# Optimization experiments

Measured on AMD Instinct MI355X. Metric: run time of the kernel, lower is better.

Reference implementation:

```python
import jax, jax.numpy as jnp
import numpy as np

H = 128  # hidden_size
DF = 6   # d_feat
T = 60
N = 8192
E = 30   # num_ind
SLOPE = 0.01  # LeakyReLU default


def leaky(v):
    return jnp.where(v >= 0, v, SLOPE * v)


def gru_layer(xs, Wih, Whh, bih, bhh):
    # xs: [T, N, D_in] -> ys: [T, N, H]
    n = xs.shape[1]
    h0 = jnp.zeros((n, H), dtype=xs.dtype)

    def step(h, xt):
        gi = xt @ Wih.T + bih          # [N, 3H]
        gh = h @ Whh.T + bhh           # [N, 3H]
        i_r, i_z, i_n = jnp.split(gi, 3, axis=1)
        h_r, h_z, h_n = jnp.split(gh, 3, axis=1)
        r = jax.nn.sigmoid(i_r + h_r)
        z = jax.nn.sigmoid(i_z + h_z)
        ncand = jnp.tanh(i_n + r * h_n)
        h_new = (1.0 - z) * ncand + z * h
        return h_new, h_new

    h_last, ys = jax.lax.scan(step, h0, xs)
    return ys, h_last


def setup_inputs() -> dict:
    key = jax.random.key(0)
    ks = jax.random.split(key, 16)
    s = 0.08
    inp = {
        "x": jax.random.normal(ks[0], (N, T, DF), dtype=jnp.float32),
        "GH": jax.random.uniform(ks[1], (N, E), dtype=jnp.float32),
        # GRU layer 0
        "Wih0": jax.random.normal(ks[2], (3 * H, DF), dtype=jnp.float32) * s,
        "Whh0": jax.random.normal(ks[3], (3 * H, H), dtype=jnp.float32) * s,
        "bih0": jax.random.normal(ks[4], (3 * H,), dtype=jnp.float32) * s,
        "bhh0": jax.random.normal(ks[5], (3 * H,), dtype=jnp.float32) * s,
        # GRU layer 1
        "Wih1": jax.random.normal(ks[6], (3 * H, H), dtype=jnp.float32) * s,
        "Whh1": jax.random.normal(ks[7], (3 * H, H), dtype=jnp.float32) * s,
        "bih1": jax.random.normal(ks[8], (3 * H,), dtype=jnp.float32) * s,
        "bhh1": jax.random.normal(ks[9], (3 * H,), dtype=jnp.float32) * s,
        # attention transformation + vector a
        "Wt": jax.random.normal(ks[10], (H, H), dtype=jnp.float32) * s,
        "bt": jax.random.normal(ks[11], (H,), dtype=jnp.float32) * s,
        "a": jax.random.normal(ks[12], (2 * H, 1), dtype=jnp.float32),
        # output heads
        "Wfc": jax.random.normal(ks[13], (H, H), dtype=jnp.float32) * s,
        "bfc": jax.random.normal(ks[14], (H,), dtype=jnp.float32) * s,
        "Wout": jax.random.normal(ks[15], (1, H), dtype=jnp.float32) * s,
        "bout": jnp.zeros((1,), dtype=jnp.float32),
    }
    return inp


def reference(x, GH, Wih0, Whh0, bih0, bhh0, Wih1, Whh1, bih1, bhh1,
              Wt, bt, a, Wfc, bfc, Wout, bout):
    # --- 2-layer GRU, batch_first; keep only last time step ---
    xs = jnp.swapaxes(x, 0, 1)                 # [T, N, DF]
    ys, _ = gru_layer(xs, Wih0, Whh0, bih0, bhh0)
    _, hidden = gru_layer(ys, Wih1, Whh1, bih1, bhh1)  # [N, H]

    # --- hyperedge aggregation ---
    hidden_agg = GH.T @ hidden                 # [E, H]

    # --- GAT-style attention, fused: score[i,j] = a1.x_i + a2.y_j ---
    xt = hidden @ Wt.T + bt                    # [N, H]
    yt = hidden_agg @ Wt.T + bt                # [E, H]
    a1 = a[:H, 0]
    a2 = a[H:, 0]
    scores = (xt @ a1)[:, None] + (yt @ a2)[None, :]   # [N, E]
    att = jax.nn.softmax(leaky(scores), axis=1)        # softmax over edges

    # --- diagonal pinv (pseudo-reciprocal); note GH.sum(1)**1/2 == sum/2 ---
    de = GH.sum(axis=0)                        # [E]
    dv = GH.sum(axis=1) / 2.0                  # [N]
    inv_de = jnp.where(de != 0, 1.0 / jnp.where(de != 0, de, 1.0), 0.0)
    inv_dv = jnp.where(dv != 0, 1.0 / jnp.where(dv != 0, dv, 1.0), 0.0)

    # H = Dv @ att @ De @ att^T @ Dv
    left = (inv_dv[:, None] * att) * inv_de[None, :]   # [N, E]
    Hmat = (left @ att.T) * inv_dv[None, :]            # [N, N]

    hidden = Hmat @ hidden + hidden
    hidden = leaky(hidden @ Wfc.T + bfc)
    out = (hidden @ Wout.T + bout).squeeze()           # [N]
    return out
```

## Files before the change

kernel.cpp:

```cpp
#include <hip/hip_runtime.h>
#include <hip/hip_fp16.h>
#include <cstddef>

#define H 128
#define E_ 30
#define T_ 60
#define DF 6

typedef unsigned int u32;
typedef __attribute__((ext_vector_type(8))) short short8;
typedef __attribute__((ext_vector_type(4))) float f32x4;

#define OFF_PACK   0
#define OFF_WFCT   79872
#define OFF_HID    96256
#define OFF_SX     1144832
#define OFF_IDV    1153024
#define OFF_AGG    1161216
#define OFF_DE     1165056
#define OFF_S      1165088
#define OFF_IDE    1168928
#define OFF_SY     1168960
#define OFF_CC     1168992
#define OFF_WV1    1169024
#define OFF_WV2    1169152
#define ZERO_CNT   7712

__device__ __forceinline__ unsigned short f2h(float f) {
    return __half_as_ushort(__float2half(f));
}

__global__ void k_pack(const float* __restrict__ Wih0, const float* __restrict__ Whh0,
                       const float* __restrict__ Wih1, const float* __restrict__ Whh1,
                       uint4* __restrict__ pack)
{
    int u = blockIdx.x * 256 + threadIdx.x;
    int lane = u & 63;
    int s = (u >> 6) % 39;
    int j = (u >> 6) / 39;
    int hc = j * 16 + (lane & 15);
    int g = lane >> 4;
    int layer, gate, kt;
    if (s < 5)       { layer = 0; gate = 0; kt = s; }
    else if (s < 10) { layer = 0; gate = 1; kt = s - 5; }
    else if (s < 14) { layer = 0; gate = 2; kt = s - 10; }
    else if (s < 15) { layer = 0; gate = 3; kt = 0; }
    else if (s < 23) { layer = 1; gate = 0; kt = s - 15; }
    else if (s < 31) { layer = 1; gate = 1; kt = s - 23; }
    else if (s < 35) { layer = 1; gate = 2; kt = s - 31; }
    else             { layer = 1; gate = 3; kt = s - 35; }

    u32 wd[4];
    for (int p = 0; p < 4; ++p) {
        unsigned short hh[2];
        for (int q = 0; q < 2; ++q) {
            int k = kt * 32 + g * 8 + p * 2 + q;
            float v = 0.f;
            if (layer == 0) {
                if (gate <= 1) {
                    int row = gate * 128 + hc;
                    if (k < 128) v = Whh0[row * 128 + k];
                    else if (k < 134) v = Wih0[row * 6 + (k - 128)];
                } else if (gate == 2) {
                    v = Whh0[(256 + hc) * 128 + k];
                } else {
                    if (k < 6) v = Wih0[(256 + hc) * 6 + k];
                }
            } else {
                if (gate <= 1) {
                    int row = gate * 128 + hc;
                    v = (k < 128) ? Wih1[row * 128 + k] : Whh1[row * 128 + (k - 128)];
                } else if (gate == 2) {
                    v = Whh1[(256 + hc) * 128 + k];
                } else {
                    v = Wih1[(256 + hc) * 128 + k];
                }
            }
            hh[q] = f2h(v);
        }
        wd[p] = (u32)hh[0] | ((u32)hh[1] << 16);
    }
    pack[(j * 39 + s) * 64 + lane] = make_uint4(wd[0], wd[1], wd[2], wd[3]);
}

__global__ void k_prep_fc(const float* __restrict__ Wfc, float* __restrict__ WfcT)
{
    int i = blockIdx.x * 256 + threadIdx.x;
    int col = i / 128, h = i % 128;
    WfcT[h * 128 + col] = Wfc[i];
}

__global__ void k_prep_wv(const float* __restrict__ Wt, const float* __restrict__ bt,
                          const float* __restrict__ a, float* __restrict__ wv1,
                          float* __restrict__ wv2, float* __restrict__ cc)
{
    int i = threadIdx.x;
    float s1 = 0.f, s2 = 0.f;
    for (int j = 0; j < H; ++j) {
        float w = Wt[(size_t)j * H + i];
        s1 += w * a[j];
        s2 += w * a[H + j];
    }
    wv1[i] = s1;
    wv2[i] = s2;
    if (i == 0) {
        float c1 = 0.f, c2 = 0.f;
        for (int j = 0; j < H; ++j) { c1 += bt[j] * a[j]; c2 += bt[j] * a[H + j]; }
        cc[0] = c1; cc[1] = c2;
    }
}

__global__ void k_zero(float* __restrict__ z)
{
    int i = blockIdx.x * 256 + threadIdx.x;
    if (i < ZERO_CNT) z[i] = 0.f;
}

#define MFMA16 __builtin_amdgcn_mfma_f32_16x16x32_f16

__global__ __launch_bounds__(512, 2) void k_gru(
    const float* __restrict__ x,
    const uint4* __restrict__ pack,
    const float* __restrict__ bih0, const float* __restrict__ bhh0,
    const float* __restrict__ bih1, const float* __restrict__ bhh1,
    float* __restrict__ hidden)
{
    extern __shared__ char smem[];
    const int tid = threadIdx.x;
    const int lane = tid & 63;
    const int j = tid >> 6;
    const int xr = lane & 15;
    const int g = lane >> 4;
    const int hc = (j << 4) + xr;
    const int n0 = blockIdx.x << 5;

    for (int c = tid; c < 32 * 60; c += 512) {
        int r = c / 60, t = c % 60;
        const float* xp = x + (size_t)(n0 + r) * (T_ * DF) + t * DF;
        u32 w0 = (u32)f2h(xp[0]) | ((u32)f2h(xp[1]) << 16);
        u32 w1 = (u32)f2h(xp[2]) | ((u32)f2h(xp[3]) << 16);
        u32 w2 = (u32)f2h(xp[4]) | ((u32)f2h(xp[5]) << 16);
        *(uint4*)(smem + 32768 + t * 512 + r * 16) = make_uint4(w0, w1, w2, 0u);
    }
    for (int i = tid; i < 384; i += 512) ((u32*)(smem + 32768 + 30720))[i] = 0u;
    for (int i = tid; i < 4096; i += 512) {
        ((u32*)smem)[i] = 0u;
        ((u32*)(smem + 16384))[i] = 0u;
    }

    uint4 wv[39];
#pragma unroll
    for (int s = 0; s < 39; ++s) wv[s] = pack[((j * 39 + s) << 6) + lane];

    const float br0 = bih0[hc] + bhh0[hc];
    const float bz0 = bih0[H + hc] + bhh0[H + hc];
    const float bgn0 = bhh0[2 * H + hc];
    const float bgi0 = bih0[2 * H + hc];
    const float br1 = bih1[hc] + bhh1[hc];
    const float bz1 = bih1[H + hc] + bhh1[H + hc];
    const float bgn1 = bhh1[2 * H + hc];
    const float bgi1 = bih1[2 * H + hc];

    float hs0[2][4] = {{0.f,0.f,0.f,0.f},{0.f,0.f,0.f,0.f}};
    float hs1[2][4] = {{0.f,0.f,0.f,0.f},{0.f,0.f,0.f,0.f}};

    const char* xbase = smem + 32768 + (g << 9) + (xr << 4);

    __syncthreads();

    for (int t = 0; t <= T_; ++t) {
        const int pr  = (t & 1) << 13;
        const int prx = pr ^ 8192;

#pragma unroll
        for (int rt = 0; rt < 2; ++rt) {
            const int R = (rt << 4) + xr;
            const int rowb = R << 8;

            uint4 f0[4];
#pragma unroll
            for (int kt = 0; kt < 4; ++kt)
                f0[kt] = *(const uint4*)(smem + prx + rowb + ((((kt << 2) | g) ^ xr) << 4));

            if (t < T_) {
                f32x4 aR = {0,0,0,0}, aZ = {0,0,0,0}, aG = {0,0,0,0}, aI = {0,0,0,0};
                uint4 fx = *(const uint4*)(xbase + (size_t)t * 512 + rt * 256);
                short8 xv = __builtin_bit_cast(short8, fx);
#pragma unroll
                for (int kt = 0; kt < 4; ++kt) {
                    short8 av = __builtin_bit_cast(short8, f0[kt]);
                    aR = MFMA16(av, __builtin_bit_cast(short8, wv[kt]), aR, 0, 0, 0);
                    aZ = MFMA16(av, __builtin_bit_cast(short8, wv[5 + kt]), aZ, 0, 0, 0);
                    aG = MFMA16(av, __builtin_bit_cast(short8, wv[10 + kt]), aG, 0, 0, 0);
                }
                aR = MFMA16(xv, __builtin_bit_cast(short8, wv[4]), aR, 0, 0, 0);
                aZ = MFMA16(xv, __builtin_bit_cast(short8, wv[9]), aZ, 0, 0, 0);
                aI = MFMA16(xv, __builtin_bit_cast(short8, wv[14]), aI, 0, 0, 0);
#pragma unroll
                for (int i = 0; i < 4; ++i) {
                    float rg = __builtin_amdgcn_rcpf(1.f + __expf(-(aR[i] + br0)));
                    float zg = __builtin_amdgcn_rcpf(1.f + __expf(-(aZ[i] + bz0)));
                    float nn = aI[i] + bgi0 + rg * (aG[i] + bgn0);
                    float e2 = __expf(2.f * nn);
                    float ng = 1.f - 2.f * __builtin_amdgcn_rcpf(e2 + 1.f);
                    float hn = ng + zg * (hs0[rt][i] - ng);
                    hs0[rt][i] = hn;
                    int Rw = (rt << 4) + (g << 2) + i;
                    *(unsigned short*)(smem + pr + (Rw << 8) + (((hc >> 3) ^ (Rw & 15)) << 4) + ((hc & 7) << 1)) = f2h(hn);
                }
            }
            __builtin_amdgcn_sched_barrier(0);

            if (t > 0) {
                f32x4 cR = {0,0,0,0}, cZ = {0,0,0,0}, cG = {0,0,0,0}, cI = {0,0,0,0};
#pragma unroll
                for (int kt = 0; kt < 4; ++kt) {
                    short8 av = __builtin_bit_cast(short8, f0[kt]);
                    cR = MFMA16(av, __builtin_bit_cast(short8, wv[15 + kt]), cR, 0, 0, 0);
                    cZ = MFMA16(av, __builtin_bit_cast(short8, wv[23 + kt]), cZ, 0, 0, 0);
                    cI = MFMA16(av, __builtin_bit_cast(short8, wv[35 + kt]), cI, 0, 0, 0);
                }
#pragma unroll
                for (int kt = 0; kt < 4; ++kt) {
                    uint4 f1 = *(const uint4*)(smem + 16384 + pr + rowb + ((((kt << 2) | g) ^ xr) << 4));
                    short8 bv = __builtin_bit_cast(short8, f1);
                    cR = MFMA16(bv, __builtin_bit_cast(short8, wv[19 + kt]), cR, 0, 0, 0);
                    cZ = MFMA16(bv, __builtin_bit_cast(short8, wv[27 + kt]), cZ, 0, 0, 0);
                    cG = MFMA16(bv, __builtin_bit_cast(short8, wv[31 + kt]), cG, 0, 0, 0);
                }
#pragma unroll
                for (int i = 0; i < 4; ++i) {
                    float rg = __builtin_amdgcn_rcpf(1.f + __expf(-(cR[i] + br1)));
                    float zg = __builtin_amdgcn_rcpf(1.f + __expf(-(cZ[i] + bz1)));
                    float nn = cI[i] + bgi1 + rg * (cG[i] + bgn1);
                    float e2 = __expf(2.f * nn);
                    float ng = 1.f - 2.f * __builtin_amdgcn_rcpf(e2 + 1.f);
                    float hn = ng + zg * (hs1[rt][i] - ng);
                    hs1[rt][i] = hn;
                    int Rw = (rt << 4) + (g << 2) + i;
                    *(unsigned short*)(smem + 16384 + prx + (Rw << 8) + (((hc >> 3) ^ (Rw & 15)) << 4) + ((hc & 7) << 1)) = f2h(hn);
                }
            }
            __builtin_amdgcn_sched_barrier(0);
        }
        __syncthreads();
    }

#pragma unroll
    for (int rt = 0; rt < 2; ++rt)
#pragma unroll
        for (int i = 0; i < 4; ++i) {
            int Rw = (rt << 4) + (g << 2) + i;
            hidden[(size_t)(n0 + Rw) * H + hc] = hs1[rt][i];
        }
}

__global__ void k_rowstats(const float* __restrict__ hidden, const float* __restrict__ GH,
                           const float* __restrict__ wv1, const float* __restrict__ cc,
                           float* __restrict__ sx, float* __restrict__ invdv)
{
    int lane = threadIdx.x & 63;
    int wv = threadIdx.x >> 6;
    int n = blockIdx.x * 4 + wv;
    float p = hidden[(size_t)n * H + lane] * wv1[lane]
            + hidden[(size_t)n * H + 64 + lane] * wv1[64 + lane];
    float g = (lane < E_) ? GH[(size_t)n * E_ + lane] : 0.f;
#pragma unroll
    for (int off = 32; off > 0; off >>= 1) {
        p += __shfl_down(p, off);
        g += __shfl_down(g, off);
    }
    if (lane == 0) {
        sx[n] = p + cc[0];
        float dv = 0.5f * g;
        invdv[n] = (dv != 0.f) ? 1.f / dv : 0.f;
    }
}

__global__ void k_agg(const float* __restrict__ hidden, const float* __restrict__ GH,
                      float* __restrict__ agg, float* __restrict__ de)
{
    int t = threadIdx.x;
    int nbase = blockIdx.x * 32;
    if (t < H) {
        float part[E_];
#pragma unroll
        for (int e = 0; e < E_; ++e) part[e] = 0.f;
        for (int r = 0; r < 32; ++r) {
            int n = nbase + r;
            float hv = hidden[(size_t)n * H + t];
#pragma unroll
            for (int e = 0; e < E_; ++e) part[e] += GH[(size_t)n * E_ + e] * hv;
        }
#pragma unroll
        for (int e = 0; e < E_; ++e) atomicAdd(&agg[e * H + t], part[e]);
    } else if (t < H + E_) {
        int e = t - H;
        float s = 0.f;
        for (int r = 0; r < 32; ++r) s += GH[(size_t)(nbase + r) * E_ + e];
        atomicAdd(&de[e], s);
    }
}

__global__ void k_sy(const float* __restrict__ agg, const float* __restrict__ wv2,
                     const float* __restrict__ cc, const float* __restrict__ de,
                     float* __restrict__ sy, float* __restrict__ invde)
{
    int e = threadIdx.x;
    if (e < E_) {
        float s = 0.f;
        for (int h = 0; h < H; ++h) s += agg[e * H + h] * wv2[h];
        sy[e] = s + cc[1];
        float d = de[e];
        invde[e] = (d != 0.f) ? 1.f / d : 0.f;
    }
}

__global__ void k_attS(const float* __restrict__ hidden, const float* __restrict__ sx,
                       const float* __restrict__ sy, const float* __restrict__ invdv,
                       float* __restrict__ S)
{
    __shared__ float att_s[32][E_];
    __shared__ float sy_s[E_];
    int t = threadIdx.x;
    if (t < E_) sy_s[t] = sy[t];
    __syncthreads();
    int nbase = blockIdx.x * 32;
    if (t < 32) {
        int n = nbase + t;
        float sxn = sx[n];
        float vv[E_];
        float m = -1e30f;
#pragma unroll
        for (int e = 0; e < E_; ++e) {
            float v = sxn + sy_s[e];
            v = (v >= 0.f) ? v : 0.01f * v;
            vv[e] = v;
            m = fmaxf(m, v);
        }
        float ss = 0.f;
#pragma unroll
        for (int e = 0; e < E_; ++e) { vv[e] = __expf(vv[e] - m); ss += vv[e]; }
        float sc = invdv[n] / ss;
#pragma unroll
        for (int e = 0; e < E_; ++e) att_s[t][e] = vv[e] * sc;
    }
    __syncthreads();
    if (t < H) {
        float part[E_];
#pragma unroll
        for (int e = 0; e < E_; ++e) part[e] = 0.f;
        for (int r = 0; r < 32; ++r) {
            float hv = hidden[(size_t)(nbase + r) * H + t];
#pragma unroll
            for (int e = 0; e < E_; ++e) part[e] += att_s[r][e] * hv;
        }
#pragma unroll
        for (int e = 0; e < E_; ++e) atomicAdd(&S[e * H + t], part[e]);
    }
}

__global__ __launch_bounds__(256) void k_final(
    const float* __restrict__ hidden, const float* __restrict__ sx,
    const float* __restrict__ sy, const float* __restrict__ invdv,
    const float* __restrict__ invde, const float* __restrict__ S,
    const float* __restrict__ WfcT, const float* __restrict__ bfc,
    const float* __restrict__ Wout, const float* __restrict__ bout,
    float* __restrict__ out)
{
    __shared__ float S_s[E_ * H];
    __shared__ float sy_s[E_], ide_s[E_];
    __shared__ float nh[4][H];
    int t = threadIdx.x;
    for (int i = t; i < E_ * H; i += 256) S_s[i] = S[i];
    if (t < E_) { sy_s[t] = sy[t]; ide_s[t] = invde[t]; }
    __syncthreads();
    int wv = t >> 6, lane = t & 63;
    float wouta = Wout[lane], woutb = Wout[64 + lane];
    float bfca = bfc[lane], bfcb = bfc[64 + lane];
    float boutv = bout[0];
    for (int it = 0; it < 8; ++it) {
        int n = blockIdx.x * 32 + it * 4 + wv;
        float sxn = sx[n];
        float idv = invdv[n];
        float vv[E_];
        float m = -1e30f;
#pragma unroll
        for (int e = 0; e < E_; ++e) {
            float v = sxn + sy_s[e];
            v = (v >= 0.f) ? v : 0.01f * v;
            vv[e] = v;
            m = fmaxf(m, v);
        }
        float ss = 0.f;
#pragma unroll
        for (int e = 0; e < E_; ++e) { vv[e] = __expf(vv[e] - m); ss += vv[e]; }
        float sc = idv / ss;
        float a0 = hidden[(size_t)n * H + lane];
        float a1 = hidden[(size_t)n * H + 64 + lane];
#pragma unroll
        for (int e = 0; e < E_; ++e) {
            float wgt = vv[e] * sc * ide_s[e];
            a0 += wgt * S_s[e * H + lane];
            a1 += wgt * S_s[e * H + 64 + lane];
        }
        nh[wv][lane] = a0;
        nh[wv][64 + lane] = a1;
        __syncthreads();
        float f0 = bfca, f1 = bfcb;
        for (int h = 0; h < H; h += 4) {
            float4 nv = *(const float4*)&nh[wv][h];
            f0 += nv.x * WfcT[(h + 0) * H + lane] + nv.y * WfcT[(h + 1) * H + lane]
                + nv.z * WfcT[(h + 2) * H + lane] + nv.w * WfcT[(h + 3) * H + lane];
            f1 += nv.x * WfcT[(h + 0) * H + 64 + lane] + nv.y * WfcT[(h + 1) * H + 64 + lane]
                + nv.z * WfcT[(h + 2) * H + 64 + lane] + nv.w * WfcT[(h + 3) * H + 64 + lane];
        }
        f0 = (f0 >= 0.f) ? f0 : 0.01f * f0;
        f1 = (f1 >= 0.f) ? f1 : 0.01f * f1;
        float op = f0 * wouta + f1 * woutb;
#pragma unroll
        for (int off = 32; off > 0; off >>= 1) op += __shfl_down(op, off);
        if (lane == 0) out[n] = op + boutv;
        __syncthreads();
    }
}

extern "C" void kernel_launch(void* const* d_in, const int* in_sizes, int n_in,
                              void* d_out, int out_size, void* d_ws, size_t ws_size,
                              hipStream_t stream)
{
    const float* x    = (const float*)d_in[0];
    const float* GH   = (const float*)d_in[1];
    const float* Wih0 = (const float*)d_in[2];
    const float* Whh0 = (const float*)d_in[3];
    const float* bih0 = (const float*)d_in[4];
    const float* bhh0 = (const float*)d_in[5];
    const float* Wih1 = (const float*)d_in[6];
    const float* Whh1 = (const float*)d_in[7];
    const float* bih1 = (const float*)d_in[8];
    const float* bhh1 = (const float*)d_in[9];
    const float* Wt   = (const float*)d_in[10];
    const float* bt   = (const float*)d_in[11];
    const float* a    = (const float*)d_in[12];
    const float* Wfc  = (const float*)d_in[13];
    const float* bfc  = (const float*)d_in[14];
    const float* Wout = (const float*)d_in[15];
    const float* bout = (const float*)d_in[16];

    float* ws    = (float*)d_ws;
    uint4* pack  = (uint4*)(ws + OFF_PACK);
    float* WfcT  = ws + OFF_WFCT;
    float* hid   = ws + OFF_HID;
    float* sx    = ws + OFF_SX;
    float* idv   = ws + OFF_IDV;
    float* agg   = ws + OFF_AGG;
    float* de    = ws + OFF_DE;
    float* S     = ws + OFF_S;
    float* ide   = ws + OFF_IDE;
    float* sy    = ws + OFF_SY;
    float* cc    = ws + OFF_CC;
    float* wv1   = ws + OFF_WV1;
    float* wv2   = ws + OFF_WV2;

    k_pack<<<78, 256, 0, stream>>>(Wih0, Whh0, Wih1, Whh1, pack);
    k_prep_fc<<<64, 256, 0, stream>>>(Wfc, WfcT);
    k_prep_wv<<<1, 128, 0, stream>>>(Wt, bt, a, wv1, wv2, cc);
    k_zero<<<31, 256, 0, stream>>>(agg);

    const size_t lds_bytes = 65024;
    (void)hipFuncSetAttribute((const void*)k_gru,
                              hipFuncAttributeMaxDynamicSharedMemorySize,
                              (int)lds_bytes);
    k_gru<<<256, 512, lds_bytes, stream>>>(x, pack, bih0, bhh0, bih1, bhh1, hid);

    k_rowstats<<<2048, 256, 0, stream>>>(hid, GH, wv1, cc, sx, idv);
    k_agg<<<256, 256, 0, stream>>>(hid, GH, agg, de);
    k_sy<<<1, 64, 0, stream>>>(agg, wv2, cc, de, sy, ide);
    k_attS<<<256, 256, 0, stream>>>(hid, sx, sy, idv, S);
    k_final<<<256, 256, 0, stream>>>(hid, sx, sy, idv, ide, S, WfcT, bfc,
                                     Wout, bout, (float*)d_out);
}
```

Before: 244.4 us.

## Pipeline GRU layers across wave roles and merge small prep/stat kernels

The GRU kernel now uses 1024 threads, split into two wave roles. One role computes layer 0 at step p together with layer 1's input projection, and the other computes layer 1 at step p-1, passing the projection through LDS. This wavefront pipeline halves the per-wave weight register footprint and overlaps the two layers' serial recurrences. The four prep kernels are merged into one launch, rowstats is folded into the aggregation kernel, and the tiny k_sy kernel is removed by recomputing sy and inv_de inside the consumers. The trade-offs are more __syncthreads per step, a larger LDS footprint, and redundant sy recomputation in every block.

```diff
diff --git a/kernel.cpp b/kernel.cpp
--- a/kernel.cpp
+++ b/kernel.cpp
@@ -19,8 +19,6 @@
 #define OFF_AGG    1161216
 #define OFF_DE     1165056
 #define OFF_S      1165088
-#define OFF_IDE    1168928
-#define OFF_SY     1168960
 #define OFF_CC     1168992
 #define OFF_WV1    1169024
 #define OFF_WV2    1169152
@@ -30,95 +28,96 @@
     return __half_as_ushort(__float2half(f));
 }
 
-__global__ void k_pack(const float* __restrict__ Wih0, const float* __restrict__ Whh0,
-                       const float* __restrict__ Wih1, const float* __restrict__ Whh1,
-                       uint4* __restrict__ pack)
+__global__ void k_prep_all(const float* __restrict__ Wih0, const float* __restrict__ Whh0,
+                           const float* __restrict__ Wih1, const float* __restrict__ Whh1,
+                           const float* __restrict__ Wfc, const float* __restrict__ Wt,
+                           const float* __restrict__ bt, const float* __restrict__ a,
+                           uint4* __restrict__ pack, float* __restrict__ WfcT,
+                           float* __restrict__ wv1, float* __restrict__ wv2,
+                           float* __restrict__ cc, float* __restrict__ zbase)
 {
-    int u = blockIdx.x * 256 + threadIdx.x;
-    int lane = u & 63;
-    int s = (u >> 6) % 39;
-    int j = (u >> 6) / 39;
-    int hc = j * 16 + (lane & 15);
-    int g = lane >> 4;
-    int layer, gate, kt;
-    if (s < 5)       { layer = 0; gate = 0; kt = s; }
-    else if (s < 10) { layer = 0; gate = 1; kt = s - 5; }
-    else if (s < 14) { layer = 0; gate = 2; kt = s - 10; }
-    else if (s < 15) { layer = 0; gate = 3; kt = 0; }
-    else if (s < 23) { layer = 1; gate = 0; kt = s - 15; }
-    else if (s < 31) { layer = 1; gate = 1; kt = s - 23; }
-    else if (s < 35) { layer = 1; gate = 2; kt = s - 31; }
-    else             { layer = 1; gate = 3; kt = s - 35; }
-
-    u32 wd[4];
-    for (int p = 0; p < 4; ++p) {
-        unsigned short hh[2];
-        for (int q = 0; q < 2; ++q) {
-            int k = kt * 32 + g * 8 + p * 2 + q;
-            float v = 0.f;
-            if (layer == 0) {
-                if (gate <= 1) {
-                    int row = gate * 128 + hc;
-                    if (k < 128) v = Whh0[row * 128 + k];
-                    else if (k < 134) v = Wih0[row * 6 + (k - 128)];
-                } else if (gate == 2) {
-                    v = Whh0[(256 + hc) * 128 + k];
+    int b = blockIdx.x;
+    if (b < 78) {
+        int u = b * 256 + threadIdx.x;
+        int lane = u & 63;
+        int s = (u >> 6) % 39;
+        int j = (u >> 6) / 39;
+        int hc = j * 16 + (lane & 15);
+        int g = lane >> 4;
+        int layer, gate, kt;
+        if (s < 5)       { layer = 0; gate = 0; kt = s; }
+        else if (s < 10) { layer = 0; gate = 1; kt = s - 5; }
+        else if (s < 14) { layer = 0; gate = 2; kt = s - 10; }
+        else if (s < 15) { layer = 0; gate = 3; kt = 0; }
+        else if (s < 23) { layer = 1; gate = 0; kt = s - 15; }
+        else if (s < 31) { layer = 1; gate = 1; kt = s - 23; }
+        else if (s < 35) { layer = 1; gate = 2; kt = s - 31; }
+        else             { layer = 1; gate = 3; kt = s - 35; }
+        u32 wd[4];
+        for (int p = 0; p < 4; ++p) {
+            unsigned short hh[2];
+            for (int q = 0; q < 2; ++q) {
+                int k = kt * 32 + g * 8 + p * 2 + q;
+                float v = 0.f;
+                if (layer == 0) {
+                    if (gate <= 1) {
+                        int row = gate * 128 + hc;
+                        if (k < 128) v = Whh0[row * 128 + k];
+                        else if (k < 134) v = Wih0[row * 6 + (k - 128)];
+                    } else if (gate == 2) {
+                        v = Whh0[(256 + hc) * 128 + k];
+                    } else {
+                        if (k < 6) v = Wih0[(256 + hc) * 6 + k];
+                    }
                 } else {
-                    if (k < 6) v = Wih0[(256 + hc) * 6 + k];
+                    if (gate <= 1) {
+                        int row = gate * 128 + hc;
+                        v = (k < 128) ? Wih1[row * 128 + k] : Whh1[row * 128 + (k - 128)];
+                    } else if (gate == 2) {
+                        v = Whh1[(256 + hc) * 128 + k];
+                    } else {
+                        v = Wih1[(256 + hc) * 128 + k];
+                    }
                 }
-            } else {
-                if (gate <= 1) {
-                    int row = gate * 128 + hc;
-                    v = (k < 128) ? Wih1[row * 128 + k] : Whh1[row * 128 + (k - 128)];
-                } else if (gate == 2) {
-                    v = Whh1[(256 + hc) * 128 + k];
-                } else {
-                    v = Wih1[(256 + hc) * 128 + k];
-                }
-            }
-            hh[q] = f2h(v);
-        }
-        wd[p] = (u32)hh[0] | ((u32)hh[1] << 16);
-    }
-    pack[(j * 39 + s) * 64 + lane] = make_uint4(wd[0], wd[1], wd[2], wd[3]);
-}
-
-__global__ void k_prep_fc(const float* __restrict__ Wfc, float* __restrict__ WfcT)
-{
-    int i = blockIdx.x * 256 + threadIdx.x;
-    int col = i / 128, h = i % 128;
-    WfcT[h * 128 + col] = Wfc[i];
-}
-
-__global__ void k_prep_wv(const float* __restrict__ Wt, const float* __restrict__ bt,
-                          const float* __restrict__ a, float* __restrict__ wv1,
-                          float* __restrict__ wv2, float* __restrict__ cc)
-{
-    int i = threadIdx.x;
-    float s1 = 0.f, s2 = 0.f;
-    for (int j = 0; j < H; ++j) {
-        float w = Wt[(size_t)j * H + i];
-        s1 += w * a[j];
-        s2 += w * a[H + j];
-    }
-    wv1[i] = s1;
-    wv2[i] = s2;
-    if (i == 0) {
-        float c1 = 0.f, c2 = 0.f;
-        for (int j = 0; j < H; ++j) { c1 += bt[j] * a[j]; c2 += bt[j] * a[H + j]; }
-        cc[0] = c1; cc[1] = c2;
-    }
-}
-
-__global__ void k_zero(float* __restrict__ z)
-{
-    int i = blockIdx.x * 256 + threadIdx.x;
-    if (i < ZERO_CNT) z[i] = 0.f;
+                hh[q] = f2h(v);
+            }
+            wd[p] = (u32)hh[0] | ((u32)hh[1] << 16);
+        }
+        pack[(j * 39 + s) * 64 + lane] = make_uint4(wd[0], wd[1], wd[2], wd[3]);
+    } else if (b < 142) {
+        int i = (b - 78) * 256 + threadIdx.x;
+        int col = i / 128, h = i % 128;
+        WfcT[h * 128 + col] = Wfc[i];
+    } else if (b == 142) {
+        int i = threadIdx.x;
+        if (i < 128) {
+            float s1 = 0.f, s2 = 0.f;
+            for (int k = 0; k < H; ++k) {
+                float w = Wt[(size_t)k * H + i];
+                s1 += w * a[k];
+                s2 += w * a[H + k];
+            }
+            wv1[i] = s1;
+            wv2[i] = s2;
+            if (i == 0) {
+                float c1 = 0.f, c2 = 0.f;
+                for (int k = 0; k < H; ++k) { c1 += bt[k] * a[k]; c2 += bt[k] * a[H + k]; }
+                cc[0] = c1; cc[1] = c2;
+            }
+        }
+    } else {
+        int i = (b - 143) * 256 + threadIdx.x;
+        if (i < ZERO_CNT) zbase[i] = 0.f;
+    }
 }
 
 #define MFMA16 __builtin_amdgcn_mfma_f32_16x16x32_f16
-
-__global__ __launch_bounds__(512, 2) void k_gru(
+#define BC8(v) __builtin_bit_cast(short8, v)
+#define GI_OFF 32768
+#define X_OFF  49664
+#define GRU_LDS 81920
+
+__global__ __launch_bounds__(1024) void k_gru(
     const float* __restrict__ x,
     const uint4* __restrict__ pack,
     const float* __restrict__ bih0, const float* __restrict__ bhh0,
@@ -128,157 +127,194 @@
     extern __shared__ char smem[];
     const int tid = threadIdx.x;
     const int lane = tid & 63;
-    const int j = tid >> 6;
+    const int w = tid >> 6;
+    const int j = w >> 1;
+    const bool roleA = (w & 1) == 0;
     const int xr = lane & 15;
     const int g = lane >> 4;
     const int hc = (j << 4) + xr;
     const int n0 = blockIdx.x << 5;
 
-    for (int c = tid; c < 32 * 60; c += 512) {
+    for (int c = tid; c < 32 * 60; c += 1024) {
         int r = c / 60, t = c % 60;
         const float* xp = x + (size_t)(n0 + r) * (T_ * DF) + t * DF;
         u32 w0 = (u32)f2h(xp[0]) | ((u32)f2h(xp[1]) << 16);
         u32 w1 = (u32)f2h(xp[2]) | ((u32)f2h(xp[3]) << 16);
         u32 w2 = (u32)f2h(xp[4]) | ((u32)f2h(xp[5]) << 16);
-        *(uint4*)(smem + 32768 + t * 512 + r * 16) = make_uint4(w0, w1, w2, 0u);
-    }
-    for (int i = tid; i < 384; i += 512) ((u32*)(smem + 32768 + 30720))[i] = 0u;
-    for (int i = tid; i < 4096; i += 512) {
-        ((u32*)smem)[i] = 0u;
-        ((u32*)(smem + 16384))[i] = 0u;
-    }
-
-    uint4 wv[39];
-#pragma unroll
-    for (int s = 0; s < 39; ++s) wv[s] = pack[((j * 39 + s) << 6) + lane];
-
-    const float br0 = bih0[hc] + bhh0[hc];
-    const float bz0 = bih0[H + hc] + bhh0[H + hc];
-    const float bgn0 = bhh0[2 * H + hc];
-    const float bgi0 = bih0[2 * H + hc];
-    const float br1 = bih1[hc] + bhh1[hc];
-    const float bz1 = bih1[H + hc] + bhh1[H + hc];
-    const float bgn1 = bhh1[2 * H + hc];
-    const float bgi1 = bih1[2 * H + hc];
-
-    float hs0[2][4] = {{0.f,0.f,0.f,0.f},{0.f,0.f,0.f,0.f}};
-    float hs1[2][4] = {{0.f,0.f,0.f,0.f},{0.f,0.f,0.f,0.f}};
-
-    const char* xbase = smem + 32768 + (g << 9) + (xr << 4);
+        *(uint4*)(smem + X_OFF + t * 512 + r * 16) = make_uint4(w0, w1, w2, 0u);
+    }
+    for (int i = tid; i < 384; i += 1024) ((u32*)(smem + X_OFF + 30720))[i] = 0u;
+    for (int i = tid; i < 8192; i += 1024) ((u32*)smem)[i] = 0u;
+
+    uint4 wv[20];
+#pragma unroll
+    for (int s = 0; s < 20; ++s) {
+        const int gsA = (s < 15) ? s : ((s < 19) ? s + 20 : 38);
+        const int gs = roleA ? gsA : (15 + s);
+        wv[s] = pack[((j * 39 + gs) << 6) + lane];
+    }
+
+    const float bR = roleA ? (bih0[hc] + bhh0[hc]) : (bih1[hc] + bhh1[hc]);
+    const float bZ = roleA ? (bih0[H + hc] + bhh0[H + hc]) : (bih1[H + hc] + bhh1[H + hc]);
+    const float bG = roleA ? bhh0[2 * H + hc] : bhh1[2 * H + hc];
+    const float bI = roleA ? bih0[2 * H + hc] : bih1[2 * H + hc];
+    const float bI2 = roleA ? bih1[2 * H + hc] : 0.f;
+
+    float hs[2][4] = {{0.f,0.f,0.f,0.f},{0.f,0.f,0.f,0.f}};
+
+    const char* xbase = smem + X_OFF + (g << 9) + (xr << 4);
 
     __syncthreads();
 
-    for (int t = 0; t <= T_; ++t) {
-        const int pr  = (t & 1) << 13;
-        const int prx = pr ^ 8192;
-
-#pragma unroll
-        for (int rt = 0; rt < 2; ++rt) {
-            const int R = (rt << 4) + xr;
-            const int rowb = R << 8;
-
-            uint4 f0[4];
-#pragma unroll
-            for (int kt = 0; kt < 4; ++kt)
-                f0[kt] = *(const uint4*)(smem + prx + rowb + ((((kt << 2) | g) ^ xr) << 4));
-
-            if (t < T_) {
-                f32x4 aR = {0,0,0,0}, aZ = {0,0,0,0}, aG = {0,0,0,0}, aI = {0,0,0,0};
-                uint4 fx = *(const uint4*)(xbase + (size_t)t * 512 + rt * 256);
-                short8 xv = __builtin_bit_cast(short8, fx);
+    for (int p = 0; p <= T_; ++p) {
+        const int h0r = ((p - 1) & 1) << 13;
+        const int h0w = (p & 1) << 13;
+        const int h1r = (p & 1) << 13;
+        const int h1w = ((p - 1) & 1) << 13;
+
+        f32x4 cR = {bR,bR,bR,bR}, cZ = {bZ,bZ,bZ,bZ}, cG = {bG,bG,bG,bG};
+        if (roleA) {
+            if (p >= 1) {
+#pragma unroll
+                for (int rt = 0; rt < 2; ++rt) {
+                    const int rowb = ((rt << 4) + xr) << 8;
+                    f32x4 aI = {bI2,bI2,bI2,bI2};
+#pragma unroll
+                    for (int kt = 0; kt < 4; ++kt) {
+                        uint4 f0 = *(const uint4*)(smem + h0r + rowb + ((((kt << 2) | g) ^ xr) << 4));
+                        aI = MFMA16(BC8(f0), BC8(wv[15 + kt]), aI, 0, 0, 0);
+                    }
+#pragma unroll
+                    for (int i = 0; i < 4; ++i) {
+                        int row = (rt << 4) + (g << 2) + i;
+                        *(float*)(smem + GI_OFF + row * 516 + (hc << 2)) = aI[i];
+                    }
+                }
+            }
+        } else if (p >= 1) {
+            const int rowb = xr << 8;
+#pragma unroll
+            for (int kt = 0; kt < 4; ++kt) {
+                uint4 f0 = *(const uint4*)(smem + h0r + rowb + ((((kt << 2) | g) ^ xr) << 4));
+                cR = MFMA16(BC8(f0), BC8(wv[kt]), cR, 0, 0, 0);
+                cZ = MFMA16(BC8(f0), BC8(wv[8 + kt]), cZ, 0, 0, 0);
+            }
+#pragma unroll
+            for (int kt = 0; kt < 4; ++kt) {
+                uint4 f1 = *(const uint4*)(smem + 16384 + h1r + rowb + ((((kt << 2) | g) ^ xr) << 4));
+                cR = MFMA16(BC8(f1), BC8(wv[4 + kt]), cR, 0, 0, 0);
+                cZ = MFMA16(BC8(f1), BC8(wv[12 + kt]), cZ, 0, 0, 0);
+                cG = MFMA16(BC8(f1), BC8(wv[16 + kt]), cG, 0, 0, 0);
+            }
+        }
+        __syncthreads();
+
+        if (roleA) {
+            if (p < T_) {
+#pragma unroll
+                for (int rt = 0; rt < 2; ++rt) {
+                    const int rowb = ((rt << 4) + xr) << 8;
+                    f32x4 aR = {bR,bR,bR,bR}, aZ = {bZ,bZ,bZ,bZ};
+                    f32x4 aG = {bG,bG,bG,bG}, aI = {bI,bI,bI,bI};
+#pragma unroll
+                    for (int kt = 0; kt < 4; ++kt) {
+                        uint4 f0 = *(const uint4*)(smem + h0r + rowb + ((((kt << 2) | g) ^ xr) << 4));
+                        aR = MFMA16(BC8(f0), BC8(wv[kt]), aR, 0, 0, 0);
+                        aZ = MFMA16(BC8(f0), BC8(wv[5 + kt]), aZ, 0, 0, 0);
+                        aG = MFMA16(BC8(f0), BC8(wv[10 + kt]), aG, 0, 0, 0);
+                    }
+                    {
+                        uint4 fx = *(const uint4*)(xbase + p * 512 + rt * 256);
+                        aR = MFMA16(BC8(fx), BC8(wv[4]), aR, 0, 0, 0);
+                        aZ = MFMA16(BC8(fx), BC8(wv[9]), aZ, 0, 0, 0);
+                        aI = MFMA16(BC8(fx), BC8(wv[14]), aI, 0, 0, 0);
+                    }
+#pragma unroll
+                    for (int i = 0; i < 4; ++i) {
+                        float da = 1.f + __expf(-aR[i]);
+                        float db = 1.f + __expf(-aZ[i]);
+                        float inv = __builtin_amdgcn_rcpf(da * db);
+                        float rg = inv * db, zg = inv * da;
+                        float nn = aI[i] + rg * aG[i];
+                        float e2 = __expf(2.f * nn);
+                        float ng = 1.f - 2.f * __builtin_amdgcn_rcpf(e2 + 1.f);
+                        float hn = ng + zg * (hs[rt][i] - ng);
+                        hs[rt][i] = hn;
+                        int Rw = (rt << 4) + (g << 2) + i;
+                        *(unsigned short*)(smem + h0w + (Rw << 8) + (((hc >> 3) ^ (Rw & 15)) << 4) + ((hc & 7) << 1)) = f2h(hn);
+                    }
+                    __builtin_amdgcn_sched_barrier(0);
+                }
+            }
+        } else if (p >= 1) {
+#pragma unroll
+            for (int i = 0; i < 4; ++i) {
+                int row = (g << 2) + i;
+                float giv = *(const float*)(smem + GI_OFF + row * 516 + (hc << 2));
+                float da = 1.f + __expf(-cR[i]);
+                float db = 1.f + __expf(-cZ[i]);
+                float inv = __builtin_amdgcn_rcpf(da * db);
+                float rg = inv * db, zg = inv * da;
+                float nn = giv + rg * cG[i];
+                float e2 = __expf(2.f * nn);
+                float ng = 1.f - 2.f * __builtin_amdgcn_rcpf(e2 + 1.f);
+                float hn = ng + zg * (hs[0][i] - ng);
+                hs[0][i] = hn;
+                *(unsigned short*)(smem + 16384 + h1w + (row << 8) + (((hc >> 3) ^ (row & 15)) << 4) + ((hc & 7) << 1)) = f2h(hn);
+            }
+            __builtin_amdgcn_sched_barrier(0);
+            {
+                const int rowb = (16 + xr) << 8;
+                f32x4 dR = {bR,bR,bR,bR}, dZ = {bZ,bZ,bZ,bZ}, dG = {bG,bG,bG,bG};
 #pragma unroll
                 for (int kt = 0; kt < 4; ++kt) {
-                    short8 av = __builtin_bit_cast(short8, f0[kt]);
-                    aR = MFMA16(av, __builtin_bit_cast(short8, wv[kt]), aR, 0, 0, 0);
-                    aZ = MFMA16(av, __builtin_bit_cast(short8, wv[5 + kt]), aZ, 0, 0, 0);
-                    aG = MFMA16(av, __builtin_bit_cast(short8, wv[10 + kt]), aG, 0, 0, 0);
+                    uint4 f0 = *(const uint4*)(smem + h0r + rowb + ((((kt << 2) | g) ^ xr) << 4));
+                    dR = MFMA16(BC8(f0), BC8(wv[kt]), dR, 0, 0, 0);
+                    dZ = MFMA16(BC8(f0), BC8(wv[8 + kt]), dZ, 0, 0, 0);
                 }
-                aR = MFMA16(xv, __builtin_bit_cast(short8, wv[4]), aR, 0, 0, 0);
-                aZ = MFMA16(xv, __builtin_bit_cast(short8, wv[9]), aZ, 0, 0, 0);
-                aI = MFMA16(xv, __builtin_bit_cast(short8, wv[14]), aI, 0, 0, 0);
+#pragma unroll
+                for (int kt = 0; kt < 4; ++kt) {
+                    uint4 f1 = *(const uint4*)(smem + 16384 + h1r + rowb + ((((kt << 2) | g) ^ xr) << 4));
+                    dR = MFMA16(BC8(f1), BC8(wv[4 + kt]), dR, 0, 0, 0);
+                    dZ = MFMA16(BC8(f1), BC8(wv[12 + kt]), dZ, 0, 0, 0);
+                    dG = MFMA16(BC8(f1), BC8(wv[16 + kt]), dG, 0, 0, 0);
+                }
 #pragma unroll
                 for (int i = 0; i < 4; ++i) {
-                    float rg = __builtin_amdgcn_rcpf(1.f + __expf(-(aR[i] + br0)));
-                    float zg = __builtin_amdgcn_rcpf(1.f + __expf(-(aZ[i] + bz0)));
-                    float nn = aI[i] + bgi0 + rg * (aG[i] + bgn0);
+                    int row = 16 + (g << 2) + i;
+                    float giv = *(const float*)(smem + GI_OFF + row * 516 + (hc << 2));
+                    float da = 1.f + __expf(-dR[i]);
+                    float db = 1.f + __expf(-dZ[i]);
+                    float inv = __builtin_amdgcn_rcpf(da * db);
+                    float rg = inv * db, zg = inv * da;
+                    float nn = giv + rg * dG[i];
                     float e2 = __expf(2.f * nn);
                     float ng = 1.f - 2.f * __builtin_amdgcn_rcpf(e2 + 1.f);
-                    float hn = ng + zg * (hs0[rt][i] - ng);
-                    hs0[rt][i] = hn;
-                    int Rw = (rt << 4) + (g << 2) + i;
-                    *(unsigned short*)(smem + pr + (Rw << 8) + (((hc >> 3) ^ (Rw & 15)) << 4) + ((hc & 7) << 1)) = f2h(hn);
+                    float hn = ng + zg * (hs[1][i] - ng);
+                    hs[1][i] = hn;
+                    *(unsigned short*)(smem + 16384 + h1w + (row << 8) + (((hc >> 3) ^ (row & 15)) << 4) + ((hc & 7) << 1)) = f2h(hn);
                 }
             }
             __builtin_amdgcn_sched_barrier(0);
-
-            if (t > 0) {
-                f32x4 cR = {0,0,0,0}, cZ = {0,0,0,0}, cG = {0,0,0,0}, cI = {0,0,0,0};
-#pragma unroll
-                for (int kt = 0; kt < 4; ++kt) {
-                    short8 av = __builtin_bit_cast(short8, f0[kt]);
-                    cR = MFMA16(av, __builtin_bit_cast(short8, wv[15 + kt]), cR, 0, 0, 0);
-                    cZ = MFMA16(av, __builtin_bit_cast(short8, wv[23 + kt]), cZ, 0, 0, 0);
-                    cI = MFMA16(av, __builtin_bit_cast(short8, wv[35 + kt]), cI, 0, 0, 0);
-                }
-#pragma unroll
-                for (int kt = 0; kt < 4; ++kt) {
-                    uint4 f1 = *(const uint4*)(smem + 16384 + pr + rowb + ((((kt << 2) | g) ^ xr) << 4));
-                    short8 bv = __builtin_bit_cast(short8, f1);
-                    cR = MFMA16(bv, __builtin_bit_cast(short8, wv[19 + kt]), cR, 0, 0, 0);
-                    cZ = MFMA16(bv, __builtin_bit_cast(short8, wv[27 + kt]), cZ, 0, 0, 0);
-                    cG = MFMA16(bv, __builtin_bit_cast(short8, wv[31 + kt]), cG, 0, 0, 0);
-                }
-#pragma unroll
-                for (int i = 0; i < 4; ++i) {
-                    float rg = __builtin_amdgcn_rcpf(1.f + __expf(-(cR[i] + br1)));
-                    float zg = __builtin_amdgcn_rcpf(1.f + __expf(-(cZ[i] + bz1)));
-                    float nn = cI[i] + bgi1 + rg * (cG[i] + bgn1);
-                    float e2 = __expf(2.f * nn);
-                    float ng = 1.f - 2.f * __builtin_amdgcn_rcpf(e2 + 1.f);
-                    float hn = ng + zg * (hs1[rt][i] - ng);
-                    hs1[rt][i] = hn;
-                    int Rw = (rt << 4) + (g << 2) + i;
-                    *(unsigned short*)(smem + 16384 + prx + (Rw << 8) + (((hc >> 3) ^ (Rw & 15)) << 4) + ((hc & 7) << 1)) = f2h(hn);
-                }
-            }
-            __builtin_amdgcn_sched_barrier(0);
         }
         __syncthreads();
     }
 
-#pragma unroll
-    for (int rt = 0; rt < 2; ++rt)
-#pragma unroll
-        for (int i = 0; i < 4; ++i) {
-            int Rw = (rt << 4) + (g << 2) + i;
-            hidden[(size_t)(n0 + Rw) * H + hc] = hs1[rt][i];
-        }
-}
-
-__global__ void k_rowstats(const float* __restrict__ hidden, const float* __restrict__ GH,
-                           const float* __restrict__ wv1, const float* __restrict__ cc,
-                           float* __restrict__ sx, float* __restrict__ invdv)
-{
-    int lane = threadIdx.x & 63;
-    int wv = threadIdx.x >> 6;
-    int n = blockIdx.x * 4 + wv;
-    float p = hidden[(size_t)n * H + lane] * wv1[lane]
-            + hidden[(size_t)n * H + 64 + lane] * wv1[64 + lane];
-    float g = (lane < E_) ? GH[(size_t)n * E_ + lane] : 0.f;
-#pragma unroll
-    for (int off = 32; off > 0; off >>= 1) {
-        p += __shfl_down(p, off);
-        g += __shfl_down(g, off);
-    }
-    if (lane == 0) {
-        sx[n] = p + cc[0];
-        float dv = 0.5f * g;
-        invdv[n] = (dv != 0.f) ? 1.f / dv : 0.f;
-    }
-}
-
-__global__ void k_agg(const float* __restrict__ hidden, const float* __restrict__ GH,
-                      float* __restrict__ agg, float* __restrict__ de)
+    if (!roleA) {
+#pragma unroll
+        for (int rt = 0; rt < 2; ++rt)
+#pragma unroll
+            for (int i = 0; i < 4; ++i) {
+                int row = (rt << 4) + (g << 2) + i;
+                hidden[(size_t)(n0 + row) * H + hc] = hs[rt][i];
+            }
+    }
+}
+
+__global__ void k_stats(const float* __restrict__ hidden, const float* __restrict__ GH,
+                        const float* __restrict__ wv1, const float* __restrict__ cc,
+                        float* __restrict__ agg, float* __restrict__ de,
+                        float* __restrict__ sx, float* __restrict__ invdv)
 {
     int t = threadIdx.x;
     int nbase = blockIdx.x * 32;
@@ -299,31 +335,40 @@
         float s = 0.f;
         for (int r = 0; r < 32; ++r) s += GH[(size_t)(nbase + r) * E_ + e];
         atomicAdd(&de[e], s);
-    }
-}
-
-__global__ void k_sy(const float* __restrict__ agg, const float* __restrict__ wv2,
-                     const float* __restrict__ cc, const float* __restrict__ de,
-                     float* __restrict__ sy, float* __restrict__ invde)
-{
-    int e = threadIdx.x;
-    if (e < E_) {
-        float s = 0.f;
-        for (int h = 0; h < H; ++h) s += agg[e * H + h] * wv2[h];
-        sy[e] = s + cc[1];
-        float d = de[e];
-        invde[e] = (d != 0.f) ? 1.f / d : 0.f;
+    } else if (t >= 192) {
+        int lane = t & 63;
+        for (int r = 0; r < 32; ++r) {
+            int n = nbase + r;
+            float p = hidden[(size_t)n * H + lane] * wv1[lane]
+                    + hidden[(size_t)n * H + 64 + lane] * wv1[64 + lane];
+            float gg = (lane < E_) ? GH[(size_t)n * E_ + lane] : 0.f;
+#pragma unroll
+            for (int off = 32; off > 0; off >>= 1) {
+                p += __shfl_down(p, off);
+                gg += __shfl_down(gg, off);
+            }
+            if (lane == 0) {
+                sx[n] = p + cc[0];
+                float dv = 0.5f * gg;
+                invdv[n] = (dv != 0.f) ? 1.f / dv : 0.f;
+            }
+        }
     }
 }
 
 __global__ void k_attS(const float* __restrict__ hidden, const float* __restrict__ sx,
-                       const float* __restrict__ sy, const float* __restrict__ invdv,
+                       const float* __restrict__ invdv, const float* __restrict__ agg,
+                       const float* __restrict__ wv2, const float* __restrict__ cc,
                        float* __restrict__ S)
 {
     __shared__ float att_s[32][E_];
     __shared__ float sy_s[E_];
     int t = threadIdx.x;
-    if (t < E_) sy_s[t] = sy[t];
+    if (t < E_) {
+        float s = 0.f;
+        for (int h = 0; h < H; ++h) s += agg[t * H + h] * wv2[h];
+        sy_s[t] = s + cc[1];
+    }
     __syncthreads();
     int nbase = blockIdx.x * 32;
     if (t < 32) {
@@ -362,10 +407,11 @@
 
 __global__ __launch_bounds__(256) void k_final(
     const float* __restrict__ hidden, const float* __restrict__ sx,
-    const float* __restrict__ sy, const float* __restrict__ invdv,
-    const float* __restrict__ invde, const float* __restrict__ S,
+    const float* __restrict__ invdv, const float* __restrict__ agg,
+    const float* __restrict__ de, const float* __restrict__ S,
     const float* __restrict__ WfcT, const float* __restrict__ bfc,
     const float* __restrict__ Wout, const float* __restrict__ bout,
+    const float* __restrict__ wv2, const float* __restrict__ cc,
     float* __restrict__ out)
 {
     __shared__ float S_s[E_ * H];
@@ -373,14 +419,20 @@
     __shared__ float nh[4][H];
     int t = threadIdx.x;
     for (int i = t; i < E_ * H; i += 256) S_s[i] = S[i];
-    if (t < E_) { sy_s[t] = sy[t]; ide_s[t] = invde[t]; }
+    if (t < E_) {
+        float s = 0.f;
+        for (int h = 0; h < H; ++h) s += agg[t * H + h] * wv2[h];
+        sy_s[t] = s + cc[1];
+        float d = de[t];
+        ide_s[t] = (d != 0.f) ? 1.f / d : 0.f;
+    }
     __syncthreads();
-    int wv = t >> 6, lane = t & 63;
+    int wvx = t >> 6, lane = t & 63;
     float wouta = Wout[lane], woutb = Wout[64 + lane];
     float bfca = bfc[lane], bfcb = bfc[64 + lane];
     float boutv = bout[0];
     for (int it = 0; it < 8; ++it) {
-        int n = blockIdx.x * 32 + it * 4 + wv;
+        int n = blockIdx.x * 32 + it * 4 + wvx;
         float sxn = sx[n];
         float idv = invdv[n];
         float vv[E_];
@@ -404,12 +456,12 @@
             a0 += wgt * S_s[e * H + lane];
             a1 += wgt * S_s[e * H + 64 + lane];
         }
-        nh[wv][lane] = a0;
-        nh[wv][64 + lane] = a1;
+        nh[wvx][lane] = a0;
+        nh[wvx][64 + lane] = a1;
         __syncthreads();
         float f0 = bfca, f1 = bfcb;
         for (int h = 0; h < H; h += 4) {
-            float4 nv = *(const float4*)&nh[wv][h];
+            float4 nv = *(const float4*)&nh[wvx][h];
             f0 += nv.x * WfcT[(h + 0) * H + lane] + nv.y * WfcT[(h + 1) * H + lane]
                 + nv.z * WfcT[(h + 2) * H + lane] + nv.w * WfcT[(h + 3) * H + lane];
             f1 += nv.x * WfcT[(h + 0) * H + 64 + lane] + nv.y * WfcT[(h + 1) * H + 64 + lane]
@@ -456,27 +508,20 @@
     float* agg   = ws + OFF_AGG;
     float* de    = ws + OFF_DE;
     float* S     = ws + OFF_S;
-    float* ide   = ws + OFF_IDE;
-    float* sy    = ws + OFF_SY;
     float* cc    = ws + OFF_CC;
     float* wv1   = ws + OFF_WV1;
     float* wv2   = ws + OFF_WV2;
 
-    k_pack<<<78, 256, 0, stream>>>(Wih0, Whh0, Wih1, Whh1, pack);
-    k_prep_fc<<<64, 256, 0, stream>>>(Wfc, WfcT);
-    k_prep_wv<<<1, 128, 0, stream>>>(Wt, bt, a, wv1, wv2, cc);
-    k_zero<<<31, 256, 0, stream>>>(agg);
-
-    const size_t lds_bytes = 65024;
+    k_prep_all<<<174, 256, 0, stream>>>(Wih0, Whh0, Wih1, Whh1, Wfc, Wt, bt, a,
+                                        pack, WfcT, wv1, wv2, cc, agg);
+
     (void)hipFuncSetAttribute((const void*)k_gru,
                               hipFuncAttributeMaxDynamicSharedMemorySize,
-                              (int)lds_bytes);
-    k_gru<<<256, 512, lds_bytes, stream>>>(x, pack, bih0, bhh0, bih1, bhh1, hid);
-
-    k_rowstats<<<2048, 256, 0, stream>>>(hid, GH, wv1, cc, sx, idv);
-    k_agg<<<256, 256, 0, stream>>>(hid, GH, agg, de);
-    k_sy<<<1, 64, 0, stream>>>(agg, wv2, cc, de, sy, ide);
-    k_attS<<<256, 256, 0, stream>>>(hid, sx, sy, idv, S);
-    k_final<<<256, 256, 0, stream>>>(hid, sx, sy, idv, ide, S, WfcT, bfc,
-                                     Wout, bout, (float*)d_out);
-}
+                              GRU_LDS);
+    k_gru<<<256, 1024, GRU_LDS, stream>>>(x, pack, bih0, bhh0, bih1, bhh1, hid);
+
+    k_stats<<<256, 256, 0, stream>>>(hid, GH, wv1, cc, agg, de, sx, idv);
+    k_attS<<<256, 256, 0, stream>>>(hid, sx, idv, agg, wv2, cc, S);
+    k_final<<<256, 256, 0, stream>>>(hid, sx, idv, agg, de, S, WfcT, bfc,
+                                     Wout, bout, wv2, cc, (float*)d_out);
+}
```

Measured after the change: 699.8 us. 2.86x slower.
